# Kernel optimization log

Hardware: AMD Instinct MI355X
Metric: run time of the kernel (lower is better)

The kernel has to match this reference:

```python
import jax, jax.numpy as jnp
import numpy as np

B, T, C, H, DH = 2, 2048, 768, 12, 64


def setup_inputs() -> dict:
    key = jax.random.key(0)
    k1, k2, k3 = jax.random.split(key, 3)
    x = jax.random.normal(k1, (B, T, C), dtype=jnp.float32)
    Wqkv = jax.random.normal(k2, (C, 3 * C), dtype=jnp.float32) * (C ** -0.5)
    Wout = jax.random.normal(k3, (C, C), dtype=jnp.float32) * (C ** -0.5)
    return {"x": x, "Wqkv": Wqkv, "Wout": Wout}


def reference(x, Wqkv, Wout):
    b, t, c = x.shape
    qkv = x @ Wqkv  # [B,T,3C]
    q, k, v = jnp.split(qkv, 3, axis=-1)
    # [B,T,C] -> [B,H,T,dh]
    q = q.reshape(b, t, H, DH).transpose(0, 2, 1, 3)
    k = k.reshape(b, t, H, DH).transpose(0, 2, 1, 3)
    v = v.reshape(b, t, H, DH).transpose(0, 2, 1, 3)
    scale = DH ** -0.5
    scores = jnp.einsum('bhqd,bhkd->bhqk', q, k) * scale  # [B,H,T,T]
    causal = jnp.tril(jnp.ones((t, t), dtype=bool))
    scores = jnp.where(causal, scores, -jnp.inf)
    weights = jax.nn.softmax(scores, axis=-1)
    # dropout p=0.0 -> identity
    out = jnp.einsum('bhqk,bhkd->bhqd', weights, v)  # [B,H,T,dh]
    out = out.transpose(0, 2, 1, 3).reshape(b, t, c)
    return out @ Wout
```

## Files before the change

kernel.cpp:

```cpp
#include <hip/hip_runtime.h>
#include <hip/hip_bf16.h>

#define Bn 2
#define Tn 2048
#define Cn 768
#define Hn 12
#define Dn 64
#define N3n 2304
#define Mn 4096

#define MASKVAL (-30000.f)
#define NITEMS 1152
#define DEFER_THR 64.f
#define L2E8 0.1803368801111204f

typedef unsigned short u16;
typedef __attribute__((ext_vector_type(8))) unsigned short ushort8_t;
typedef __attribute__((ext_vector_type(8))) short bf16x8;
typedef __attribute__((ext_vector_type(4))) float f32x4;
typedef __attribute__((address_space(1))) unsigned int* gas1_t;
typedef __attribute__((address_space(3))) unsigned int* las3_t;

__device__ __forceinline__ float bf2f(u16 u) {
  union { unsigned int i; float f; } v; v.i = ((unsigned int)u) << 16; return v.f;
}
__device__ __forceinline__ u16 f2bf(float f) {
  union { float f; unsigned int i; } v; v.f = f;
  return (u16)((v.i + 0x7fffu + ((v.i >> 16) & 1u)) >> 16);
}

#define E(qt, s0, s1, ck) (((qt) << 24) | ((s0) << 16) | ((s1) << 8) | (ck))
__constant__ unsigned int SCHED[48] = {
    E(31, 0, 16, 0), E(31, 16, 32, 1), E(30, 0, 16, 0), E(15, 0, 16, 2),
    E(30, 16, 31, 1), E(29, 0, 15, 0), E(29, 15, 30, 1), E(28, 0, 15, 0), E(14, 0, 15, 2),
    E(28, 15, 29, 1), E(27, 0, 14, 0), E(27, 14, 28, 1), E(26, 0, 14, 0), E(13, 0, 14, 2),
    E(26, 14, 27, 1), E(25, 0, 13, 0), E(25, 13, 26, 1), E(24, 0, 13, 0), E(12, 0, 13, 2),
    E(24, 13, 25, 1), E(23, 0, 12, 0), E(23, 12, 24, 1), E(22, 0, 12, 0), E(11, 0, 12, 2),
    E(22, 12, 23, 1), E(21, 0, 11, 0), E(21, 11, 22, 1), E(20, 0, 11, 0), E(10, 0, 11, 2),
    E(20, 11, 21, 1), E(19, 0, 10, 0), E(19, 10, 20, 1), E(18, 0, 10, 0), E(9, 0, 10, 2),
    E(18, 10, 19, 1), E(17, 0, 9, 0), E(17, 9, 18, 1), E(16, 0, 9, 0), E(8, 0, 9, 2),
    E(16, 9, 17, 1), E(7, 0, 8, 2),
    E(6, 0, 7, 2), E(5, 0, 6, 2), E(4, 0, 5, 2), E(3, 0, 4, 2), E(2, 0, 3, 2),
    E(1, 0, 2, 2), E(0, 0, 1, 2)};

__global__ __launch_bounds__(256) void prep_kernel(const float* __restrict__ x,
                                                   const float* __restrict__ Wqkv,
                                                   const float* __restrict__ Wout,
                                                   u16* __restrict__ xb,
                                                   u16* __restrict__ WqkvT,
                                                   u16* __restrict__ WoutT,
                                                   int* __restrict__ counter) {
  __shared__ u16 t[32][33];
  const int bx = blockIdx.x;
  const int tid = threadIdx.x;
  if (bx < 3072) {
    if (bx == 0 && tid == 0) *counter = 0;
    const int i = (bx * 256 + tid) * 4;
    float4 v = *(const float4*)(x + i);
    ushort4 s;
    s.x = f2bf(v.x); s.y = f2bf(v.y); s.z = f2bf(v.z); s.w = f2bf(v.w);
    *(ushort4*)(xb + i) = s;
  } else {
    const int idx = bx - 3072;
    const int gx = idx % 96, gy = idx / 96;
    const bool isA = gx < (N3n / 32);
    const float* in = isA ? Wqkv : Wout;
    u16* out = isA ? WqkvT : WoutT;
    const int Cc = isA ? N3n : Cn;
    const int c0 = (isA ? gx : gx - N3n / 32) * 32;
    const int r0 = gy * 32;
    const int tx = tid & 31, ty = tid >> 5;
#pragma unroll
    for (int i = 0; i < 4; i++)
      t[ty * 4 + i][tx] = f2bf(in[(size_t)(r0 + ty * 4 + i) * Cc + c0 + tx]);
    __syncthreads();
#pragma unroll
    for (int i = 0; i < 4; i++)
      out[(size_t)(c0 + ty * 4 + i) * Cn + r0 + tx] = t[tx][ty * 4 + i];
  }
}

#define BK 64

template <int EPI>
__global__ __launch_bounds__(256) void mfma_gemm(const u16* __restrict__ A,
                                                 const u16* __restrict__ BT,
                                                 u16* __restrict__ Q,
                                                 u16* __restrict__ Kd,
                                                 u16* __restrict__ VT,
                                                 float* __restrict__ out) {
  __shared__ __align__(16) u16 Ash[128 * BK];
  __shared__ __align__(16) u16 Bsh[128 * BK];
  const int tid = threadIdx.x;
  const int wv = tid >> 6, lane = tid & 63;
  const int lo = lane & 15, quad = lane >> 4;
  const int wm = wv & 1, wn = wv >> 1;

  const int nwg = gridDim.x * gridDim.y;
  const int cpx = nwg >> 3;
  const int lid = blockIdx.y * gridDim.x + blockIdx.x;
  const int swz = (lid & 7) * cpx + (lid >> 3);
  const int n0 = (swz % gridDim.x) * 128;
  const int m0 = (swz / gridDim.x) * 128;

  const int srow = lane >> 3;
  const int scol = (lane & 7) << 3;

  f32x4 acc[4][4];
#pragma unroll
  for (int i = 0; i < 4; i++)
#pragma unroll
    for (int j = 0; j < 4; j++) acc[i][j] = f32x4{0.f, 0.f, 0.f, 0.f};

  for (int k0 = 0; k0 < Cn; k0 += BK) {
    __syncthreads();
#pragma unroll
    for (int c = 0; c < 4; c++) {
      const int rb = (wv << 5) + (c << 3);
      const int gr = rb + srow;
      __builtin_amdgcn_global_load_lds(
          (gas1_t)(A + (size_t)(m0 + gr) * Cn + k0 + scol),
          (las3_t)(&Ash[rb * BK]), 16, 0, 0);
      __builtin_amdgcn_global_load_lds(
          (gas1_t)(BT + (size_t)(n0 + gr) * Cn + k0 + scol),
          (las3_t)(&Bsh[rb * BK]), 16, 0, 0);
    }
    __syncthreads();

    bf16x8 af[4][2], bfr[4][2];
#pragma unroll
    for (int t = 0; t < 4; t++) {
#pragma unroll
      for (int s = 0; s < 2; s++) {
        af[t][s]  = *(const bf16x8*)&Ash[(wm * 64 + t * 16 + lo) * BK + s * 32 + (quad << 3)];
        bfr[t][s] = *(const bf16x8*)&Bsh[(wn * 64 + t * 16 + lo) * BK + s * 32 + (quad << 3)];
      }
    }
#pragma unroll
    for (int mt = 0; mt < 4; mt++)
#pragma unroll
      for (int nt = 0; nt < 4; nt++) {
        acc[mt][nt] = __builtin_amdgcn_mfma_f32_16x16x32_bf16(af[mt][0], bfr[nt][0],
                                                              acc[mt][nt], 0, 0, 0);
        acc[mt][nt] = __builtin_amdgcn_mfma_f32_16x16x32_bf16(af[mt][1], bfr[nt][1],
                                                              acc[mt][nt], 0, 0, 0);
      }
  }

  if (EPI == 0) {
    const int which = n0 / Cn;
    const int h = ((n0 % Cn) >> 6) + wn;
    const int bb = m0 >> 11;
    const int t_base = (m0 & (Tn - 1)) + wm * 64;
    if (which < 2) {
      u16* dst = ((which == 0) ? Q : Kd) + (size_t)(bb * Hn + h) * Tn * Dn;
#pragma unroll
      for (int mt = 0; mt < 4; mt++)
#pragma unroll
        for (int nt = 0; nt < 4; nt++)
#pragma unroll
          for (int r = 0; r < 4; r++) {
            const int t = t_base + mt * 16 + (quad << 2) + r;
            dst[(size_t)t * Dn + nt * 16 + lo] = f2bf(acc[mt][nt][r]);
          }
    } else {
      u16* dst = VT + (size_t)(bb * Hn + h) * Dn * Tn;
#pragma unroll
      for (int mt = 0; mt < 4; mt++)
#pragma unroll
        for (int nt = 0; nt < 4; nt++) {
          const int t = t_base + mt * 16 + (quad << 2);
          const int d = nt * 16 + lo;
          ushort4 st;
          st.x = f2bf(acc[mt][nt][0]); st.y = f2bf(acc[mt][nt][1]);
          st.z = f2bf(acc[mt][nt][2]); st.w = f2bf(acc[mt][nt][3]);
          *(ushort4*)&dst[(size_t)d * Tn + t] = st;
        }
    }
  } else {
#pragma unroll
    for (int mt = 0; mt < 4; mt++)
#pragma unroll
      for (int nt = 0; nt < 4; nt++)
#pragma unroll
        for (int r = 0; r < 4; r++) {
          const int m = m0 + wm * 64 + mt * 16 + (quad << 2) + r;
          out[(size_t)m * Cn + n0 + wn * 64 + nt * 16 + lo] = acc[mt][nt][r];
        }
  }
}

#define TILE_W (64 * 64)

__global__ __launch_bounds__(256) void attn_kernel(const u16* __restrict__ Q,
                                                   const u16* __restrict__ K,
                                                   const u16* __restrict__ VT,
                                                   u16* __restrict__ O,
                                                   int* __restrict__ counter,
                                                   float* __restrict__ po,
                                                   float* __restrict__ pm,
                                                   float* __restrict__ pl) {
  __shared__ __align__(16) u16 Ksh[2 * TILE_W];
  __shared__ __align__(16) u16 Vsh[2 * TILE_W];
  __shared__ __align__(16) u16 Pw[4][16 * 64];
  int* sip = (int*)&Ksh[TILE_W];

  const int tid = threadIdx.x;
  const int wv = tid >> 6, lane = tid & 63;
  const int lo = lane & 15, quad = lane >> 4;
  const int lo7 = lo & 7;
  const int ck0 = (quad ^ lo7) << 3;
  const int ck1 = ck0 ^ 32;
  const int sr = tid >> 3;
  const int sc = (tid & 7) << 3;
  const int scw = (((tid & 7) ^ (sr & 7)) << 3);

  for (;;) {
    if (tid == 0) *sip = atomicAdd(counter, 1);
    __syncthreads();
    const int item = *sip;
    if (item >= NITEMS) return;

    const unsigned int e = SCHED[item / 24];
    const int qt = e >> 24, ck = e & 255;
    const int jstart = ((e >> 16) & 255) << 6;
    const int jend   = ((e >> 8) & 255) << 6;
    const int q0 = qt << 6;
    const int hb = item % 24;
    const int h = hb % 12, b = hb / 12;
    const size_t base = (size_t)(b * Hn + h) * Tn * Dn;
    const size_t vtb  = (size_t)(b * Hn + h) * Dn * Tn;

    const u16* qp = Q + base + (size_t)(q0 + (wv << 4) + lo) * Dn + (quad << 3);
    const bf16x8 aq0 = *(const bf16x8*)qp;
    const bf16x8 aq1 = *(const bf16x8*)(qp + 32);

    f32x4 o[4] = {f32x4{0,0,0,0}, f32x4{0,0,0,0}, f32x4{0,0,0,0}, f32x4{0,0,0,0}};
    float m1 = MASKVAL;
    float l1 = 0.f;

#pragma unroll
    for (int it = 0; it < 2; it++) {
      const int r = sr + it * 32;
      *(ushort8_t*)&Ksh[r * 64 + scw] =
          *(const ushort8_t*)(K + base + (size_t)(jstart + r) * Dn + sc);
      *(ushort8_t*)&Vsh[r * 64 + scw] =
          *(const ushort8_t*)(VT + vtb + (size_t)r * Tn + jstart + sc);
    }
    __syncthreads();

    int cur = 0;
    const int qrel = (wv << 4) + lo;

    for (int j0 = jstart; j0 < jend; j0 += 64) {
      const bool hasnext = (j0 + 64 < jend);

      ushort8_t kr[2], vr[2];
      if (hasnext) {
#pragma unroll
        for (int it = 0; it < 2; it++) {
          const int r = sr + it * 32;
          kr[it] = *(const ushort8_t*)(K + base + (size_t)(j0 + 64 + r) * Dn + sc);
          vr[it] = *(const ushort8_t*)(VT + vtb + (size_t)r * Tn + j0 + 64 + sc);
        }
      }

      const u16* Kb_ = &Ksh[cur * TILE_W];
      const u16* Vb_ = &Vsh[cur * TILE_W];

      f32x4 s[4];
#pragma unroll
      for (int nt = 0; nt < 4; nt++) {
        const bf16x8 bk0 = *(const bf16x8*)(&Kb_[(nt * 16 + lo) * 64 + ck0]);
        const bf16x8 bk1 = *(const bf16x8*)(&Kb_[(nt * 16 + lo) * 64 + ck1]);
        f32x4 a = {0.f, 0.f, 0.f, 0.f};
        a = __builtin_amdgcn_mfma_f32_16x16x32_bf16(bk0, aq0, a, 0, 0, 0);
        a = __builtin_amdgcn_mfma_f32_16x16x32_bf16(bk1, aq1, a, 0, 0, 0);
        s[nt] = a;
      }

      if (j0 == q0) {
#pragma unroll
        for (int nt = 0; nt < 4; nt++)
#pragma unroll
          for (int r = 0; r < 4; r++) {
            const int kv = nt * 16 + (quad << 2) + r;
            if (kv > qrel) s[nt][r] = MASKVAL;
          }
      }

      float mx = fmaxf(s[0][0], s[0][1]);
      mx = fmaxf(fmaxf(mx, s[0][2]), s[0][3]);
      mx = fmaxf(fmaxf(mx, s[1][0]), s[1][1]);
      mx = fmaxf(fmaxf(mx, s[1][2]), s[1][3]);
      mx = fmaxf(fmaxf(mx, s[2][0]), s[2][1]);
      mx = fmaxf(fmaxf(mx, s[2][2]), s[2][3]);
      mx = fmaxf(fmaxf(mx, s[3][0]), s[3][1]);
      mx = fmaxf(fmaxf(mx, s[3][2]), s[3][3]);
      const float pmax = mx;

      if (!__all(pmax <= m1 + DEFER_THR)) {
        float mr = fmaxf(pmax, __shfl_xor(pmax, 16));
        mr = fmaxf(mr, __shfl_xor(mr, 32));
        const float mnew = fmaxf(m1, mr);
        const float alpha = __builtin_amdgcn_exp2f(L2E8 * (m1 - mnew));
        m1 = mnew;
        l1 *= alpha;
        float ar[4];
#pragma unroll
        for (int r = 0; r < 4; r++) ar[r] = __shfl(alpha, (quad << 2) + r);
#pragma unroll
        for (int nt = 0; nt < 4; nt++)
#pragma unroll
          for (int r = 0; r < 4; r++) o[nt][r] *= ar[r];
      }

      const float mb2 = L2E8 * m1;
      float sum = 0.f;
#pragma unroll
      for (int nt = 0; nt < 4; nt++)
#pragma unroll
        for (int r = 0; r < 4; r++) {
          const float p = __builtin_amdgcn_exp2f(L2E8 * s[nt][r] - mb2);
          s[nt][r] = p;
          sum += p;
        }
      l1 += sum;

      u16* pw = Pw[wv];
#pragma unroll
      for (int nt = 0; nt < 4; nt++) {
        ushort4 pk;
        pk.x = f2bf(s[nt][0]); pk.y = f2bf(s[nt][1]);
        pk.z = f2bf(s[nt][2]); pk.w = f2bf(s[nt][3]);
        const int pc = (((2 * nt + (quad >> 1)) ^ lo7) << 3) + ((quad & 1) << 2);
        *(ushort4*)&pw[lo * 64 + pc] = pk;
      }
      const bf16x8 pa0 = *(const bf16x8*)(&pw[lo * 64 + ck0]);
      const bf16x8 pa1 = *(const bf16x8*)(&pw[lo * 64 + ck1]);

#pragma unroll
      for (int nt = 0; nt < 4; nt++) {
        const bf16x8 bv0 = *(const bf16x8*)(&Vb_[(nt * 16 + lo) * 64 + ck0]);
        const bf16x8 bv1 = *(const bf16x8*)(&Vb_[(nt * 16 + lo) * 64 + ck1]);
        o[nt] = __builtin_amdgcn_mfma_f32_16x16x32_bf16(pa0, bv0, o[nt], 0, 0, 0);
        o[nt] = __builtin_amdgcn_mfma_f32_16x16x32_bf16(pa1, bv1, o[nt], 0, 0, 0);
      }

      if (hasnext) {
        const int nb = cur ^ 1;
#pragma unroll
        for (int it = 0; it < 2; it++) {
          const int r = sr + it * 32;
          *(ushort8_t*)&Ksh[nb * TILE_W + r * 64 + scw] = kr[it];
          *(ushort8_t*)&Vsh[nb * TILE_W + r * 64 + scw] = vr[it];
        }
      }
      __syncthreads();
      cur ^= 1;
    }

    float lt = l1;
    lt += __shfl_xor(lt, 16);
    lt += __shfl_xor(lt, 32);
    const float linv = 1.f / lt;
    float ir[4];
#pragma unroll
    for (int r = 0; r < 4; r++) ir[r] = __shfl(linv, (quad << 2) + r);

    if (ck == 2) {
#pragma unroll
      for (int nt = 0; nt < 4; nt++)
#pragma unroll
        for (int r = 0; r < 4; r++) {
          const int row = q0 + (wv << 4) + (quad << 2) + r;
          const int col = h * 64 + nt * 16 + lo;
          O[(size_t)(b * Tn + row) * Cn + col] = f2bf(o[nt][r] * ir[r]);
        }
    } else {
      const int st = hb * 16 + (qt - 16);
      const int pidx = st * 2 + ck;
      float* pO = po + ((size_t)pidx << 12);
#pragma unroll
      for (int nt = 0; nt < 4; nt++)
#pragma unroll
        for (int r = 0; r < 4; r++)
          pO[((wv << 4) + (quad << 2) + r) * 64 + nt * 16 + lo] = o[nt][r] * ir[r];
      if (quad == 0) {
        pm[pidx * 64 + (wv << 4) + lo] = m1;
        pl[pidx * 64 + (wv << 4) + lo] = lt;
      }
    }
  }
}

__global__ __launch_bounds__(256) void combine_kernel(const float* __restrict__ po,
                                                      const float* __restrict__ pm,
                                                      const float* __restrict__ pl,
                                                      u16* __restrict__ O) {
  const int st = blockIdx.x;
  const int hb = st >> 4;
  const int h = hb % 12, b = hb / 12;
  const int q0 = (16 + (st & 15)) << 6;
  const int tid = threadIdx.x;
  const int row = tid >> 2, cc0 = (tid & 3) << 4;
  const float* pa = po + (((size_t)st * 2) << 12) + row * 64 + cc0;
  const float* pb = pa + 4096;
  const float ma = pm[st * 128 + row],      la = pl[st * 128 + row];
  const float mb = pm[st * 128 + 64 + row], lb = pl[st * 128 + 64 + row];
  const float mm = fmaxf(ma, mb);
  float wa = la * __builtin_amdgcn_exp2f(L2E8 * (ma - mm));
  float wb = lb * __builtin_amdgcn_exp2f(L2E8 * (mb - mm));
  const float wi = 1.f / (wa + wb);
  wa *= wi; wb *= wi;
  u16* Orow = O + (size_t)(b * Tn + q0 + row) * Cn + h * 64 + cc0;
#pragma unroll
  for (int i = 0; i < 16; i += 4) {
    const float4 va = *(const float4*)(pa + i);
    const float4 vb = *(const float4*)(pb + i);
    ushort4 s4;
    s4.x = f2bf(wa * va.x + wb * vb.x);
    s4.y = f2bf(wa * va.y + wb * vb.y);
    s4.z = f2bf(wa * va.z + wb * vb.z);
    s4.w = f2bf(wa * va.w + wb * vb.w);
    *(ushort4*)(Orow + i) = s4;
  }
}

extern "C" void kernel_launch(void* const* d_in, const int* in_sizes, int n_in,
                              void* d_out, int out_size, void* d_ws, size_t ws_size,
                              hipStream_t stream) {
  const float* x    = (const float*)d_in[0];
  const float* Wqkv = (const float*)d_in[1];
  const float* Wout = (const float*)d_in[2];
  float* out = (float*)d_out;

  const size_t per = (size_t)Bn * Hn * Tn * Dn;
  u16* xb    = (u16*)d_ws;
  u16* WqkvT = xb + (size_t)Mn * Cn;
  u16* WoutT = WqkvT + (size_t)N3n * Cn;
  u16* Qb    = WoutT + (size_t)Cn * Cn;
  u16* Kb    = Qb + per;
  u16* VTb   = Kb + per;
  u16* attn  = VTb + per;
  int* counter = (int*)(attn + (size_t)Mn * Cn);
  float* po = (float*)(counter + 512);
  float* pm = po + (size_t)768 * 4096;
  float* pl = pm + (size_t)768 * 64;

  prep_kernel<<<dim3(3072 + 2304), 256, 0, stream>>>(x, Wqkv, Wout, xb, WqkvT,
                                                     WoutT, counter);
  mfma_gemm<0><<<dim3(N3n / 128, Mn / 128), 256, 0, stream>>>(xb, WqkvT, Qb, Kb, VTb, nullptr);
  attn_kernel<<<dim3(1024), 256, 0, stream>>>(Qb, Kb, VTb, attn, counter, po, pm, pl);
  combine_kernel<<<dim3(384), 256, 0, stream>>>(po, pm, pl, attn);
  mfma_gemm<1><<<dim3(Cn / 128, Mn / 128), 256, 0, stream>>>(attn, WoutT, nullptr, nullptr, nullptr, out);
}
```

Before: 184.4 us.

## Keep P in registers via permlane32 swap and permute V shared-memory layout

```diff
diff --git a/kernel.cpp b/kernel.cpp
--- a/kernel.cpp
+++ b/kernel.cpp
@@ -18,6 +18,7 @@
 typedef __attribute__((ext_vector_type(8))) unsigned short ushort8_t;
 typedef __attribute__((ext_vector_type(8))) short bf16x8;
 typedef __attribute__((ext_vector_type(4))) float f32x4;
+typedef __attribute__((ext_vector_type(2))) unsigned int uint2v;
 typedef __attribute__((address_space(1))) unsigned int* gas1_t;
 typedef __attribute__((address_space(3))) unsigned int* las3_t;
 
@@ -202,7 +203,6 @@
                                                    float* __restrict__ pl) {
   __shared__ __align__(16) u16 Ksh[2 * TILE_W];
   __shared__ __align__(16) u16 Vsh[2 * TILE_W];
-  __shared__ __align__(16) u16 Pw[4][16 * 64];
   int* sip = (int*)&Ksh[TILE_W];
 
   const int tid = threadIdx.x;
@@ -214,6 +214,9 @@
   const int sr = tid >> 3;
   const int sc = (tid & 7) << 3;
   const int scw = (((tid & 7) ^ (sr & 7)) << 3);
+  const int t7 = tid & 7;
+  const int vb0 = (((t7 & 6) ^ (sr & 7)) << 3) + ((t7 & 1) << 2);
+  const int vb1 = ((((t7 & 6) | 1) ^ (sr & 7)) << 3) + ((t7 & 1) << 2);
 
   for (;;) {
     if (tid == 0) *sip = atomicAdd(counter, 1);
@@ -244,8 +247,10 @@
       const int r = sr + it * 32;
       *(ushort8_t*)&Ksh[r * 64 + scw] =
           *(const ushort8_t*)(K + base + (size_t)(jstart + r) * Dn + sc);
-      *(ushort8_t*)&Vsh[r * 64 + scw] =
-          *(const ushort8_t*)(VT + vtb + (size_t)r * Tn + jstart + sc);
+      union { ushort8_t u; uint2v hh[2]; } vv;
+      vv.u = *(const ushort8_t*)(VT + vtb + (size_t)r * Tn + jstart + sc);
+      *(uint2v*)&Vsh[r * 64 + vb0] = vv.hh[0];
+      *(uint2v*)&Vsh[r * 64 + vb1] = vv.hh[1];
     }
     __syncthreads();
 
@@ -327,24 +332,31 @@
         }
       l1 += sum;
 
-      u16* pw = Pw[wv];
-#pragma unroll
-      for (int nt = 0; nt < 4; nt++) {
-        ushort4 pk;
-        pk.x = f2bf(s[nt][0]); pk.y = f2bf(s[nt][1]);
-        pk.z = f2bf(s[nt][2]); pk.w = f2bf(s[nt][3]);
-        const int pc = (((2 * nt + (quad >> 1)) ^ lo7) << 3) + ((quad & 1) << 2);
-        *(ushort4*)&pw[lo * 64 + pc] = pk;
-      }
-      const bf16x8 pa0 = *(const bf16x8*)(&pw[lo * 64 + ck0]);
-      const bf16x8 pa1 = *(const bf16x8*)(&pw[lo * 64 + ck1]);
+      unsigned int A0, B0, A1, B1, A2, B2, A3, B3;
+      asm("v_cvt_pk_bf16_f32 %0, %1, %2" : "=v"(A0) : "v"(s[0][0]), "v"(s[0][1]));
+      asm("v_cvt_pk_bf16_f32 %0, %1, %2" : "=v"(B0) : "v"(s[0][2]), "v"(s[0][3]));
+      asm("v_cvt_pk_bf16_f32 %0, %1, %2" : "=v"(A1) : "v"(s[1][0]), "v"(s[1][1]));
+      asm("v_cvt_pk_bf16_f32 %0, %1, %2" : "=v"(B1) : "v"(s[1][2]), "v"(s[1][3]));
+      asm("v_cvt_pk_bf16_f32 %0, %1, %2" : "=v"(A2) : "v"(s[2][0]), "v"(s[2][1]));
+      asm("v_cvt_pk_bf16_f32 %0, %1, %2" : "=v"(B2) : "v"(s[2][2]), "v"(s[2][3]));
+      asm("v_cvt_pk_bf16_f32 %0, %1, %2" : "=v"(A3) : "v"(s[3][0]), "v"(s[3][1]));
+      asm("v_cvt_pk_bf16_f32 %0, %1, %2" : "=v"(B3) : "v"(s[3][2]), "v"(s[3][3]));
+      const auto rA01 = __builtin_amdgcn_permlane32_swap(A0, A1, false, false);
+      const auto rB01 = __builtin_amdgcn_permlane32_swap(B0, B1, false, false);
+      const auto rA23 = __builtin_amdgcn_permlane32_swap(A2, A3, false, false);
+      const auto rB23 = __builtin_amdgcn_permlane32_swap(B2, B3, false, false);
+      union { unsigned int w[4]; bf16x8 v; } pa0u, pa1u;
+      pa0u.w[0] = rA01[0]; pa0u.w[1] = rB01[0];
+      pa0u.w[2] = rA01[1]; pa0u.w[3] = rB01[1];
+      pa1u.w[0] = rA23[0]; pa1u.w[1] = rB23[0];
+      pa1u.w[2] = rA23[1]; pa1u.w[3] = rB23[1];
 
 #pragma unroll
       for (int nt = 0; nt < 4; nt++) {
         const bf16x8 bv0 = *(const bf16x8*)(&Vb_[(nt * 16 + lo) * 64 + ck0]);
         const bf16x8 bv1 = *(const bf16x8*)(&Vb_[(nt * 16 + lo) * 64 + ck1]);
-        o[nt] = __builtin_amdgcn_mfma_f32_16x16x32_bf16(pa0, bv0, o[nt], 0, 0, 0);
-        o[nt] = __builtin_amdgcn_mfma_f32_16x16x32_bf16(pa1, bv1, o[nt], 0, 0, 0);
+        o[nt] = __builtin_amdgcn_mfma_f32_16x16x32_bf16(pa0u.v, bv0, o[nt], 0, 0, 0);
+        o[nt] = __builtin_amdgcn_mfma_f32_16x16x32_bf16(pa1u.v, bv1, o[nt], 0, 0, 0);
       }
 
       if (hasnext) {
@@ -353,7 +365,10 @@
         for (int it = 0; it < 2; it++) {
           const int r = sr + it * 32;
           *(ushort8_t*)&Ksh[nb * TILE_W + r * 64 + scw] = kr[it];
-          *(ushort8_t*)&Vsh[nb * TILE_W + r * 64 + scw] = vr[it];
+          union { ushort8_t u; uint2v hh[2]; } vv;
+          vv.u = vr[it];
+          *(uint2v*)&Vsh[nb * TILE_W + r * 64 + vb0] = vv.hh[0];
+          *(uint2v*)&Vsh[nb * TILE_W + r * 64 + vb1] = vv.hh[1];
         }
       }
       __syncthreads();
```

After: 181.6 us. About the same (-1.5%).
